# Optimization experiments

Measured on AMD Instinct MI355X. Metric: run time of the kernel, lower is better.

## Reference

```python
import jax, jax.numpy as jnp
import numpy as np

B, S = 1, 1863
D_MODEL, H = 1024, 16
HD = D_MODEL // H  # 64
MAX_X, MAX_Y, MAX_Z = 32, 32, 8
BASE = 10000.0
MAX_DXY, MAX_DZ = 30, 8
N_PAIRS = HD // 2
PX = N_PAIRS // 3  # 10
PY = N_PAIRS // 3  # 10
PZ = N_PAIRS - PX - PY  # 12


def _rotate_half(x):
    # (x0,x1,x2,x3,...) -> (-x1,x0,-x3,x2,...)
    x1 = x[..., ::2]
    x2 = x[..., 1::2]
    return jnp.stack((-x2, x1), axis=-1).reshape(x.shape)


def _rope_tables(max_pos, dim):
    inv = 1.0 / (BASE ** (np.arange(0, dim, 2, dtype=np.float32) / dim))
    f = np.outer(np.arange(max_pos, dtype=np.float32), inv)
    return jnp.asarray(np.cos(f)), jnp.asarray(np.sin(f))


def setup_inputs() -> dict:
    key = jax.random.key(0)
    ks = jax.random.split(key, 8)
    x = jax.random.normal(ks[0], (B, S, D_MODEL), dtype=jnp.float32)
    Wqkv = jax.random.normal(ks[1], (3 * D_MODEL, D_MODEL), dtype=jnp.float32) * 0.02
    Wout = jax.random.normal(ks[2], (D_MODEL, D_MODEL), dtype=jnp.float32) * 0.02
    bias_x = jax.random.normal(ks[3], (2 * MAX_DXY + 1, H), dtype=jnp.float32) * 0.02
    bias_y = jax.random.normal(ks[4], (2 * MAX_DXY + 1, H), dtype=jnp.float32) * 0.02
    bias_z = jax.random.normal(ks[5], (2 * MAX_DZ + 1, H), dtype=jnp.float32) * 0.02
    pos_xyz = jax.random.randint(ks[6], (B, S, 3), 0, 32, dtype=jnp.int32)
    return {"x": x, "Wqkv": Wqkv, "Wout": Wout, "bias_x": bias_x,
            "bias_y": bias_y, "bias_z": bias_z, "pos_xyz": pos_xyz}


def _apply_rope3d(q, k, pos_xyz):
    cx, sx = _rope_tables(MAX_X, 2 * PX)
    cy, sy = _rope_tables(MAX_Y, 2 * PY)
    cz, sz = _rope_tables(MAX_Z, 2 * PZ)
    xp = jnp.clip(pos_xyz[..., 0], 0, MAX_X - 1)
    yp = jnp.clip(pos_xyz[..., 1], 0, MAX_Y - 1)
    zp = jnp.clip(pos_xyz[..., 2], 0, MAX_Z - 1)
    # [B,S,head_dim] after repeat-interleave(2) per axis, then concat
    cos = jnp.concatenate([jnp.repeat(cx[xp], 2, axis=-1),
                           jnp.repeat(cy[yp], 2, axis=-1),
                           jnp.repeat(cz[zp], 2, axis=-1)], axis=-1)[:, :, None, :]
    sin = jnp.concatenate([jnp.repeat(sx[xp], 2, axis=-1),
                           jnp.repeat(sy[yp], 2, axis=-1),
                           jnp.repeat(sz[zp], 2, axis=-1)], axis=-1)[:, :, None, :]
    q_rot = q * cos + _rotate_half(q) * sin
    k_rot = k * cos + _rotate_half(k) * sin
    return q_rot, k_rot


def reference(x, Wqkv, Wout, bias_x, bias_y, bias_z, pos_xyz):
    b, s, _ = x.shape
    qkv = x @ Wqkv.T  # [B,S,3*D]
    q, k, v = jnp.split(qkv, 3, axis=-1)
    q = q.reshape(b, s, H, HD)
    k = k.reshape(b, s, H, HD)
    v = v.reshape(b, s, H, HD)
    q, k = _apply_rope3d(q, k, pos_xyz)
    scores = jnp.einsum('bqhd,bkhd->bhqk', q, k) * (HD ** -0.5)
    # 3D relative position bias
    px_, py_, pz_ = pos_xyz[..., 0], pos_xyz[..., 1], pos_xyz[..., 2]
    dx = jnp.clip(px_[:, :, None] - px_[:, None, :], -MAX_DXY, MAX_DXY) + MAX_DXY
    dy = jnp.clip(py_[:, :, None] - py_[:, None, :], -MAX_DXY, MAX_DXY) + MAX_DXY
    dz = jnp.clip(pz_[:, :, None] - pz_[:, None, :], -MAX_DZ, MAX_DZ) + MAX_DZ
    bias = (bias_x[dx] + bias_y[dy] + bias_z[dz]).transpose(0, 3, 1, 2)  # [B,H,S,S]
    scores = scores + bias
    causal = jnp.tril(jnp.ones((s, s), dtype=bool))
    scores = jnp.where(causal, scores, -jnp.inf)
    attn = jax.nn.softmax(scores, axis=-1)
    out = jnp.einsum('bhqk,bkhd->bqhd', attn, v).reshape(b, s, D_MODEL)
    return out @ Wout.T
```

## Files before the change

kernel.cpp:

```cpp
#include <hip/hip_runtime.h>

typedef __bf16 bf16;
typedef __bf16 bf16x2 __attribute__((ext_vector_type(2)));
typedef __bf16 bf16x4 __attribute__((ext_vector_type(4)));
typedef __bf16 bf16x8 __attribute__((ext_vector_type(8)));
typedef float  f32x4  __attribute__((ext_vector_type(4)));

#define S_LEN 1863
#define S_PAD 1920
#define DM 1024
#define NH 16
#define HDIM 64
#define AUGD 160
#define QKV_STRIDE 3072
#define NQT128 15
#define CHUNK 4
#define MAXC 8
#define NQMULTI 13
#define NCHUNK_HEAD 64

#define MFMA_BF16 __builtin_amdgcn_mfma_f32_16x16x32_bf16

__constant__ int QT_BASE[15] = {0, 1, 2, 4, 6, 9, 12, 16, 20, 25, 30, 36, 42, 49, 56};

__global__ void cvt3(const float* __restrict__ a, bf16* __restrict__ oa, int na4,
                     const float* __restrict__ b, bf16* __restrict__ ob, int nb4,
                     const float* __restrict__ c, bf16* __restrict__ oc, int nc4) {
  int j = blockIdx.x * blockDim.x + threadIdx.x;
  const float* s; bf16* d;
  if (j < na4) { s = a; d = oa; }
  else {
    j -= na4;
    if (j < nb4) { s = b; d = ob; }
    else { j -= nb4; if (j >= nc4) return; s = c; d = oc; }
  }
  float4 v = ((const float4*)s)[j];
  bf16x4 o;
  o[0] = (bf16)v.x; o[1] = (bf16)v.y; o[2] = (bf16)v.z; o[3] = (bf16)v.w;
  ((bf16x4*)d)[j] = o;
}

template <typename T>
__global__ __launch_bounds__(256) void gemm_bt(const bf16* __restrict__ A,
                                               const bf16* __restrict__ B,
                                               T* __restrict__ C,
                                               int M, int N, int K) {
  __shared__ bf16 As[128][40];
  __shared__ bf16 Bs[64][40];
  const int t = threadIdx.x;
  const int w = t >> 6, l = t & 63;
  const int quad = l >> 4, l16 = l & 15;
  const int wm = w >> 1, wn = w & 1;
  const int bm = blockIdx.y * 128, bn = blockIdx.x * 64;

  f32x4 acc[4][2];
#pragma unroll
  for (int mi = 0; mi < 4; ++mi)
#pragma unroll
    for (int ni = 0; ni < 2; ++ni) acc[mi][ni] = 0;

  const int srow = t >> 2;
  const int sk8  = (t & 3) * 8;

  for (int k0 = 0; k0 < K; k0 += 32) {
    bf16x8 a0 = *(const bf16x8*)&A[(size_t)min(bm + srow,      M - 1) * K + k0 + sk8];
    bf16x8 a1 = *(const bf16x8*)&A[(size_t)min(bm + srow + 64, M - 1) * K + k0 + sk8];
    bf16x8 b0 = *(const bf16x8*)&B[(size_t)(bn + srow) * K + k0 + sk8];
    __syncthreads();
    *(bf16x8*)&As[srow][sk8]      = a0;
    *(bf16x8*)&As[srow + 64][sk8] = a1;
    *(bf16x8*)&Bs[srow][sk8]      = b0;
    __syncthreads();

    bf16x8 af[4], bfr[2];
#pragma unroll
    for (int mi = 0; mi < 4; ++mi) af[mi]  = *(bf16x8*)&As[wm * 64 + mi * 16 + l16][quad * 8];
#pragma unroll
    for (int ni = 0; ni < 2; ++ni) bfr[ni] = *(bf16x8*)&Bs[wn * 32 + ni * 16 + l16][quad * 8];
#pragma unroll
    for (int mi = 0; mi < 4; ++mi)
#pragma unroll
      for (int ni = 0; ni < 2; ++ni)
        acc[mi][ni] = MFMA_BF16(af[mi], bfr[ni], acc[mi][ni], 0, 0, 0);
  }

#pragma unroll
  for (int mi = 0; mi < 4; ++mi)
#pragma unroll
    for (int r = 0; r < 4; ++r) {
      int m = bm + wm * 64 + mi * 16 + quad * 4 + r;
      if (m < M) {
#pragma unroll
        for (int ni = 0; ni < 2; ++ni)
          C[(size_t)m * N + bn + wn * 32 + ni * 16 + l16] = (T)acc[mi][ni][r];
      }
    }
}

__global__ __launch_bounds__(256) void gemm_bt64(const bf16* __restrict__ A,
                                                 const bf16* __restrict__ B,
                                                 float* __restrict__ C,
                                                 int M, int N, int K) {
  __shared__ bf16 As[64][40];
  __shared__ bf16 Bs[64][40];
  const int t = threadIdx.x;
  const int w = t >> 6, l = t & 63;
  const int quad = l >> 4, l16 = l & 15;
  const int wm = w >> 1, wn = w & 1;
  const int bm = blockIdx.y * 64, bn = blockIdx.x * 64;

  f32x4 acc[2][2];
#pragma unroll
  for (int mi = 0; mi < 2; ++mi)
#pragma unroll
    for (int ni = 0; ni < 2; ++ni) acc[mi][ni] = 0;

  const int srow = t >> 2;
  const int sk8  = (t & 3) * 8;

  for (int k0 = 0; k0 < K; k0 += 32) {
    bf16x8 a0 = *(const bf16x8*)&A[(size_t)min(bm + srow, M - 1) * K + k0 + sk8];
    bf16x8 b0 = *(const bf16x8*)&B[(size_t)(bn + srow) * K + k0 + sk8];
    __syncthreads();
    *(bf16x8*)&As[srow][sk8] = a0;
    *(bf16x8*)&Bs[srow][sk8] = b0;
    __syncthreads();

    bf16x8 af[2], bfr[2];
#pragma unroll
    for (int mi = 0; mi < 2; ++mi) af[mi]  = *(bf16x8*)&As[wm * 32 + mi * 16 + l16][quad * 8];
#pragma unroll
    for (int ni = 0; ni < 2; ++ni) bfr[ni] = *(bf16x8*)&Bs[wn * 32 + ni * 16 + l16][quad * 8];
#pragma unroll
    for (int mi = 0; mi < 2; ++mi)
#pragma unroll
      for (int ni = 0; ni < 2; ++ni)
        acc[mi][ni] = MFMA_BF16(af[mi], bfr[ni], acc[mi][ni], 0, 0, 0);
  }

#pragma unroll
  for (int mi = 0; mi < 2; ++mi)
#pragma unroll
    for (int r = 0; r < 4; ++r) {
      int m = bm + wm * 32 + mi * 16 + quad * 4 + r;
      if (m < M) {
#pragma unroll
        for (int ni = 0; ni < 2; ++ni)
          C[(size_t)m * N + bn + wn * 32 + ni * 16 + l16] = acc[mi][ni][r];
      }
    }
}

__global__ __launch_bounds__(256) void pack_all(const bf16* __restrict__ qkv,
                                                const int* __restrict__ pos,
                                                const float* __restrict__ bxg,
                                                const float* __restrict__ byg,
                                                const float* __restrict__ bzg,
                                                bf16* __restrict__ Qa,
                                                bf16* __restrict__ Ka,
                                                bf16* __restrict__ Vt) {
  const int st = blockIdx.x, h = blockIdx.y;
  const int t = threadIdx.x;
  __shared__ float bxs[61], bys[61], bzs[17];
  __shared__ float vtile[64][68];

  if (t < 61) { bxs[t] = bxg[t * NH + h]; bys[t] = byg[t * NH + h]; }
  if (t < 17) bzs[t] = bzg[t * NH + h];

  for (int i = t; i < 1024; i += 256) {
    int row = i >> 4, c4 = (i & 15) * 4;
    int sg = min(st * 64 + row, S_LEN - 1);
    bf16x4 v = *(const bf16x4*)&qkv[(size_t)sg * QKV_STRIDE + 2 * DM + h * HDIM + c4];
    *(float4*)&vtile[row][c4] = make_float4((float)v[0], (float)v[1], (float)v[2], (float)v[3]);
  }
  __syncthreads();

  for (int i = t; i < 2048; i += 256) {
    const int sl = i >> 5, sub = i & 31;
    const int s = st * 64 + sl;
    const int sc = min(s, S_LEN - 1);
    const int px = pos[sc * 3 + 0], py = pos[sc * 3 + 1], pz = pos[sc * 3 + 2];
    int j, P, pp;
    if (sub < 10)      { j = sub;      P = 10; pp = min(max(px, 0), 31); }
    else if (sub < 20) { j = sub - 10; P = 10; pp = min(max(py, 0), 31); }
    else               { j = sub - 20; P = 12; pp = min(max(pz, 0), 7);  }
    const float inv = __expf(-(float)j / (float)P * 9.210340371976184f);
    const float ang = (float)pp * inv;
    float sn, cs;
    __sincosf(ang, &sn, &cs);
    const size_t base = (size_t)sc * QKV_STRIDE + h * HDIM + 2 * sub;
    bf16x2 q2 = *(const bf16x2*)&qkv[base];
    bf16x2 k2 = *(const bf16x2*)&qkv[base + DM];
    float q0 = (float)q2[0], q1 = (float)q2[1];
    float k0 = (float)k2[0], k1 = (float)k2[1];
    const size_t rb = ((size_t)h * S_PAD + s) * AUGD;
    bf16x2 oq, ok;
    oq[0] = (bf16)((q0 * cs - q1 * sn) * 0.125f);
    oq[1] = (bf16)((q1 * cs + q0 * sn) * 0.125f);
    ok[0] = (bf16)(k0 * cs - k1 * sn);
    ok[1] = (bf16)(k1 * cs + k0 * sn);
    *(bf16x2*)&Qa[rb + 2 * sub] = oq;
    *(bf16x2*)&Ka[rb + 2 * sub] = ok;

    const int ix = min(max(px - sub, -30), 30) + 30;
    const int iy = min(max(py - sub, -30), 30) + 30;
    const int iz = min(max(pz - sub, -8), 8) + 8;
    Qa[rb + 64 + sub]  = (bf16)bxs[ix];
    Qa[rb + 96 + sub]  = (bf16)bys[iy];
    Qa[rb + 128 + sub] = (bf16)bzs[iz];
    Ka[rb + 64 + sub]  = (bf16)(sub == px ? 1.0f : 0.0f);
    Ka[rb + 96 + sub]  = (bf16)(sub == py ? 1.0f : 0.0f);
    Ka[rb + 128 + sub] = (bf16)(sub == pz ? 1.0f : 0.0f);
  }

  for (int i = t; i < 1024; i += 256) {
    int d = i >> 4, s4 = (i & 15) * 4;
    bf16x4 o;
    o[0] = (bf16)vtile[s4 + 0][d];
    o[1] = (bf16)vtile[s4 + 1][d];
    o[2] = (bf16)vtile[s4 + 2][d];
    o[3] = (bf16)vtile[s4 + 3][d];
    *(bf16x4*)&Vt[((size_t)h * HDIM + d) * S_PAD + st * 64 + s4] = o;
  }
}

__global__ __launch_bounds__(256) void attn_split(const bf16* __restrict__ Qa,
                                                  const bf16* __restrict__ Ka,
                                                  const bf16* __restrict__ Vt,
                                                  bf16* __restrict__ outb,
                                                  float* __restrict__ Opart,
                                                  float* __restrict__ lpart) {
  const int b = blockIdx.x;
  const int h = b >> 6;
  const int id = b & 63;
  int qt = 14;
  while (QT_BASE[qt] > id) --qt;
  const int c = id - QT_BASE[qt];
  const int chain = 2 * qt + 2;
  const int k0 = c * CHUNK;
  const int kend = min(k0 + CHUNK, chain);

  const int t = threadIdx.x, w = t >> 6, l = t & 63;
  const int quad = l >> 4, l16 = l & 15;

  __shared__ bf16 Ks[64][168];
  __shared__ bf16 Vs[64][72];
  __shared__ bf16 Ps[4][16][72];

  bf16x8 aq[2][5];
  int ig[2][4];
#pragma unroll
  for (int mi = 0; mi < 2; ++mi) {
    const int qrow = qt * 128 + w * 32 + mi * 16 + l16;
    const bf16* qp = &Qa[((size_t)h * S_PAD + qrow) * AUGD + quad * 8];
#pragma unroll
    for (int sg = 0; sg < 5; ++sg) aq[mi][sg] = *(const bf16x8*)(qp + sg * 32);
#pragma unroll
    for (int r = 0; r < 4; ++r) ig[mi][r] = qt * 128 + w * 32 + mi * 16 + quad * 4 + r;
  }

  f32x4 O[2][4];
#pragma unroll
  for (int mi = 0; mi < 2; ++mi)
#pragma unroll
    for (int di = 0; di < 4; ++di) O[mi][di] = 0;
  float lacc[2][4] = {};

  for (int kt = k0; kt < kend; ++kt) {
    __syncthreads();
    for (int i = t; i < 1280; i += 256) {
      int row = i / 20, c8 = (i - row * 20) * 8;
      *(bf16x8*)&Ks[row][c8] =
          *(const bf16x8*)&Ka[((size_t)h * S_PAD + kt * 64 + row) * AUGD + c8];
    }
    for (int i = t; i < 512; i += 256) {
      int row = i >> 3, c8 = (i & 7) * 8;
      *(bf16x8*)&Vs[row][c8] =
          *(const bf16x8*)&Vt[((size_t)h * HDIM + row) * S_PAD + kt * 64 + c8];
    }
    __syncthreads();

    f32x4 sf[2][4];
#pragma unroll
    for (int ni = 0; ni < 4; ++ni) {
      bf16x8 bk[5];
      const bf16* kp = &Ks[ni * 16 + l16][quad * 8];
#pragma unroll
      for (int sg = 0; sg < 5; ++sg) bk[sg] = *(const bf16x8*)(kp + sg * 32);
#pragma unroll
      for (int mi = 0; mi < 2; ++mi) {
        f32x4 z = {0.f, 0.f, 0.f, 0.f};
#pragma unroll
        for (int sg = 0; sg < 5; ++sg) z = MFMA_BF16(aq[mi][sg], bk[sg], z, 0, 0, 0);
        sf[mi][ni] = z;
      }
    }

#pragma unroll
    for (int mi = 0; mi < 2; ++mi) {
      const bool msk = (kt * 64 + 63) > (qt * 128 + w * 32 + mi * 16);
#pragma unroll
      for (int ni = 0; ni < 4; ++ni) {
        const int jg = kt * 64 + ni * 16 + l16;
#pragma unroll
        for (int r = 0; r < 4; ++r) {
          float p = __expf(sf[mi][ni][r]);
          if (msk && jg > ig[mi][r]) p = 0.f;
          lacc[mi][r] += p;
          Ps[w][quad * 4 + r][ni * 16 + l16] = (bf16)p;
        }
      }
      bf16x8 ap0 = *(bf16x8*)&Ps[w][l16][quad * 8];
      bf16x8 ap1 = *(bf16x8*)&Ps[w][l16][32 + quad * 8];
#pragma unroll
      for (int di = 0; di < 4; ++di) {
        bf16x8 bv0 = *(bf16x8*)&Vs[di * 16 + l16][quad * 8];
        bf16x8 bv1 = *(bf16x8*)&Vs[di * 16 + l16][32 + quad * 8];
        O[mi][di] = MFMA_BF16(ap0, bv0, O[mi][di], 0, 0, 0);
        O[mi][di] = MFMA_BF16(ap1, bv1, O[mi][di], 0, 0, 0);
      }
    }
  }

#pragma unroll
  for (int mi = 0; mi < 2; ++mi)
#pragma unroll
    for (int r = 0; r < 4; ++r) {
      float v = lacc[mi][r];
      v += __shfl_xor(v, 1);
      v += __shfl_xor(v, 2);
      v += __shfl_xor(v, 4);
      v += __shfl_xor(v, 8);
      lacc[mi][r] = v;
    }

  if (k0 == 0 && kend == chain) {
#pragma unroll
    for (int mi = 0; mi < 2; ++mi)
#pragma unroll
      for (int r = 0; r < 4; ++r) {
        const int row = ig[mi][r];
        if (row < S_LEN) {
          const float inv = 1.0f / lacc[mi][r];
#pragma unroll
          for (int di = 0; di < 4; ++di)
            outb[(size_t)row * DM + h * HDIM + di * 16 + l16] = (bf16)(O[mi][di][r] * inv);
        }
      }
  } else {
    float* ob = Opart + (((size_t)h * NQMULTI + (qt - 2)) * MAXC + c) * 8192;
#pragma unroll
    for (int mi = 0; mi < 2; ++mi)
#pragma unroll
      for (int r = 0; r < 4; ++r) {
        const int row32 = w * 32 + mi * 16 + quad * 4 + r;
#pragma unroll
        for (int di = 0; di < 4; ++di)
          ob[row32 * 64 + di * 16 + l16] = O[mi][di][r];
      }
    if (l16 == 0) {
      float* lb = lpart + (((size_t)h * NQMULTI + (qt - 2)) * MAXC + c) * 128;
#pragma unroll
      for (int mi = 0; mi < 2; ++mi)
#pragma unroll
        for (int r = 0; r < 4; ++r) lb[w * 32 + mi * 16 + quad * 4 + r] = lacc[mi][r];
    }
  }
}

__global__ __launch_bounds__(256) void attn_combine(const float* __restrict__ Opart,
                                                    const float* __restrict__ lpart,
                                                    bf16* __restrict__ outb) {
  const int qt = blockIdx.x + 2;
  const int h = blockIdx.y;
  const int t = threadIdx.x;
  const int row = t >> 1, half = t & 1;
  const int nchunk = (2 * qt + 5) >> 2;
  float4 acc[8];
#pragma unroll
  for (int j = 0; j < 8; ++j) acc[j] = make_float4(0.f, 0.f, 0.f, 0.f);
  float lsum = 0.f;
  const size_t pb = ((size_t)h * NQMULTI + (qt - 2)) * MAXC;
  for (int cc = 0; cc < nchunk; ++cc) {
    const float4* p4 = (const float4*)(Opart + (pb + cc) * 8192 + row * 64 + half * 32);
#pragma unroll
    for (int j = 0; j < 8; ++j) {
      float4 v = p4[j];
      acc[j].x += v.x; acc[j].y += v.y; acc[j].z += v.z; acc[j].w += v.w;
    }
    lsum += lpart[(pb + cc) * 128 + row];
  }
  const int s = qt * 128 + row;
  if (s < S_LEN) {
    const float inv = 1.0f / lsum;
    bf16* op = outb + (size_t)s * DM + h * HDIM + half * 32;
#pragma unroll
    for (int j = 0; j < 8; ++j) {
      bf16x4 o;
      o[0] = (bf16)(acc[j].x * inv);
      o[1] = (bf16)(acc[j].y * inv);
      o[2] = (bf16)(acc[j].z * inv);
      o[3] = (bf16)(acc[j].w * inv);
      *(bf16x4*)&op[j * 4] = o;
    }
  }
}

extern "C" void kernel_launch(void* const* d_in, const int* in_sizes, int n_in,
                              void* d_out, int out_size, void* d_ws, size_t ws_size,
                              hipStream_t stream) {
  const float* x    = (const float*)d_in[0];
  const float* Wqkv = (const float*)d_in[1];
  const float* Wout = (const float*)d_in[2];
  const float* bx   = (const float*)d_in[3];
  const float* by   = (const float*)d_in[4];
  const float* bz   = (const float*)d_in[5];
  const int*   pos  = (const int*)d_in[6];
  float* out = (float*)d_out;

  char* ws = (char*)d_ws;
  float* Opart = (float*)ws;
  bf16* xb    = (bf16*)ws;
  bf16* wqkvb = xb + (size_t)S_LEN * DM;
  bf16* qkvb  = wqkvb + (size_t)QKV_STRIDE * DM;
  ws += (size_t)NH * NQMULTI * MAXC * 8192 * 4;
  bf16* woutb = (bf16*)ws;   ws += (size_t)DM * DM * 2;
  bf16* Qaug  = (bf16*)ws;   ws += (size_t)NH * S_PAD * AUGD * 2;
  bf16* Kaug  = (bf16*)ws;   ws += (size_t)NH * S_PAD * AUGD * 2;
  bf16* Vtb   = (bf16*)ws;   ws += (size_t)NH * S_PAD * HDIM * 2;
  bf16* attnb = (bf16*)ws;   ws += (size_t)S_LEN * DM * 2;
  float* lpart = (float*)ws; ws += (size_t)NH * NQMULTI * MAXC * 128 * 4;

  const int na4 = S_LEN * DM / 4, nb4 = QKV_STRIDE * DM / 4, nc4 = DM * DM / 4;
  const int ntot = na4 + nb4 + nc4;
  cvt3<<<dim3((ntot + 255) / 256), 256, 0, stream>>>(x, xb, na4, Wqkv, wqkvb, nb4, Wout, woutb, nc4);
  gemm_bt<bf16><<<dim3(QKV_STRIDE / 64, NQT128), 256, 0, stream>>>(
      xb, wqkvb, qkvb, S_LEN, QKV_STRIDE, DM);
  pack_all<<<dim3(S_PAD / 64, NH), 256, 0, stream>>>(qkvb, pos, bx, by, bz, Qaug, Kaug, Vtb);
  attn_split<<<dim3(NH * NCHUNK_HEAD), 256, 0, stream>>>(Qaug, Kaug, Vtb, attnb, Opart, lpart);
  attn_combine<<<dim3(NQMULTI, NH), 256, 0, stream>>>(Opart, lpart, attnb);
  gemm_bt64<<<dim3(DM / 64, (S_LEN + 63) / 64), 256, 0, stream>>>(
      attnb, woutb, out, S_LEN, DM, DM);
}
```

Measured before the change: 188.3 us.

## Load K tiles via direct global-to-LDS DMA and reorder attention block schedule

Pads the augmented K layout in global memory to the LDS row stride (168) so each 64-row K tile is one contiguous block. That block is then copied with global_load_lds 16-byte DMA instead of register-staged vector loads. Block indices are also remapped so heads interleave and the longest query tiles launch first, to improve load balance. Costs include slightly larger K storage and reliance on correct sync for the DMA writes; the unused padding columns (160 to 167) are never written by pack_all.

Measured after the change: 174.3 us. -7.4%, faster.

```diff
diff --git a/kernel.cpp b/kernel.cpp
--- a/kernel.cpp
+++ b/kernel.cpp
@@ -12,6 +12,7 @@
 #define NH 16
 #define HDIM 64
 #define AUGD 160
+#define KA_STR 168
 #define QKV_STRIDE 3072
 #define NQT128 15
 #define CHUNK 4
@@ -22,6 +23,12 @@
 #define MFMA_BF16 __builtin_amdgcn_mfma_f32_16x16x32_bf16
 
 __constant__ int QT_BASE[15] = {0, 1, 2, 4, 6, 9, 12, 16, 20, 25, 30, 36, 42, 49, 56};
+
+__device__ __forceinline__ void dma16(const bf16* g, bf16* l) {
+  __builtin_amdgcn_global_load_lds(
+      (const __attribute__((address_space(1))) unsigned int*)g,
+      (__attribute__((address_space(3))) unsigned int*)l, 16, 0, 0);
+}
 
 __global__ void cvt3(const float* __restrict__ a, bf16* __restrict__ oa, int na4,
                      const float* __restrict__ b, bf16* __restrict__ ob, int nb4,
@@ -193,24 +200,25 @@
     bf16x2 k2 = *(const bf16x2*)&qkv[base + DM];
     float q0 = (float)q2[0], q1 = (float)q2[1];
     float k0 = (float)k2[0], k1 = (float)k2[1];
-    const size_t rb = ((size_t)h * S_PAD + s) * AUGD;
+    const size_t qb = ((size_t)h * S_PAD + s) * AUGD;
+    const size_t kb = ((size_t)h * S_PAD + s) * KA_STR;
     bf16x2 oq, ok;
     oq[0] = (bf16)((q0 * cs - q1 * sn) * 0.125f);
     oq[1] = (bf16)((q1 * cs + q0 * sn) * 0.125f);
     ok[0] = (bf16)(k0 * cs - k1 * sn);
     ok[1] = (bf16)(k1 * cs + k0 * sn);
-    *(bf16x2*)&Qa[rb + 2 * sub] = oq;
-    *(bf16x2*)&Ka[rb + 2 * sub] = ok;
+    *(bf16x2*)&Qa[qb + 2 * sub] = oq;
+    *(bf16x2*)&Ka[kb + 2 * sub] = ok;
 
     const int ix = min(max(px - sub, -30), 30) + 30;
     const int iy = min(max(py - sub, -30), 30) + 30;
     const int iz = min(max(pz - sub, -8), 8) + 8;
-    Qa[rb + 64 + sub]  = (bf16)bxs[ix];
-    Qa[rb + 96 + sub]  = (bf16)bys[iy];
-    Qa[rb + 128 + sub] = (bf16)bzs[iz];
-    Ka[rb + 64 + sub]  = (bf16)(sub == px ? 1.0f : 0.0f);
-    Ka[rb + 96 + sub]  = (bf16)(sub == py ? 1.0f : 0.0f);
-    Ka[rb + 128 + sub] = (bf16)(sub == pz ? 1.0f : 0.0f);
+    Qa[qb + 64 + sub]  = (bf16)bxs[ix];
+    Qa[qb + 96 + sub]  = (bf16)bys[iy];
+    Qa[qb + 128 + sub] = (bf16)bzs[iz];
+    Ka[kb + 64 + sub]  = (bf16)(sub == px ? 1.0f : 0.0f);
+    Ka[kb + 96 + sub]  = (bf16)(sub == py ? 1.0f : 0.0f);
+    Ka[kb + 128 + sub] = (bf16)(sub == pz ? 1.0f : 0.0f);
   }
 
   for (int i = t; i < 1024; i += 256) {
@@ -231,8 +239,8 @@
                                                   float* __restrict__ Opart,
                                                   float* __restrict__ lpart) {
   const int b = blockIdx.x;
-  const int h = b >> 6;
-  const int id = b & 63;
+  const int h = b & 15;
+  const int id = 63 - (b >> 4);
   int qt = 14;
   while (QT_BASE[qt] > id) --qt;
   const int c = id - QT_BASE[qt];
@@ -243,7 +251,7 @@
   const int t = threadIdx.x, w = t >> 6, l = t & 63;
   const int quad = l >> 4, l16 = l & 15;
 
-  __shared__ bf16 Ks[64][168];
+  __shared__ bf16 Ks[64][KA_STR];
   __shared__ bf16 Vs[64][72];
   __shared__ bf16 Ps[4][16][72];
 
@@ -266,12 +274,17 @@
     for (int di = 0; di < 4; ++di) O[mi][di] = 0;
   float lacc[2][4] = {};
 
+  bf16* KsF = &Ks[0][0];
+
   for (int kt = k0; kt < kend; ++kt) {
     __syncthreads();
-    for (int i = t; i < 1280; i += 256) {
-      int row = i / 20, c8 = (i - row * 20) * 8;
-      *(bf16x8*)&Ks[row][c8] =
-          *(const bf16x8*)&Ka[((size_t)h * S_PAD + kt * 64 + row) * AUGD + c8];
+    {
+      const bf16* gtile = &Ka[((size_t)h * S_PAD + kt * 64) * KA_STR];
+#pragma unroll
+      for (int seg = 0; seg < 6; ++seg) {
+        int sidx = w + seg * 4;
+        if (sidx < 21) dma16(gtile + sidx * 512 + l * 8, KsF + sidx * 512);
+      }
     }
     for (int i = t; i < 512; i += 256) {
       int row = i >> 3, c8 = (i & 7) * 8;
@@ -426,7 +439,7 @@
   ws += (size_t)NH * NQMULTI * MAXC * 8192 * 4;
   bf16* woutb = (bf16*)ws;   ws += (size_t)DM * DM * 2;
   bf16* Qaug  = (bf16*)ws;   ws += (size_t)NH * S_PAD * AUGD * 2;
-  bf16* Kaug  = (bf16*)ws;   ws += (size_t)NH * S_PAD * AUGD * 2;
+  bf16* Kaug  = (bf16*)ws;   ws += (size_t)NH * S_PAD * KA_STR * 2;
   bf16* Vtb   = (bf16*)ws;   ws += (size_t)NH * S_PAD * HDIM * 2;
   bf16* attnb = (bf16*)ws;   ws += (size_t)S_LEN * DM * 2;
   float* lpart = (float*)ws; ws += (size_t)NH * NQMULTI * MAXC * 128 * 4;
```
